# Performance work log

Hardware: AMD Instinct MI355X
Metric: run time of the kernel (lower is better)

Reference implementation:

```python
import jax, jax.numpy as jnp
import numpy as np

SPIKE_THRESHOLD = 0.5
SURROGATE_ALPHA = 4.0
EPS = 1e-8

B, S, D, F = 32, 8192, 64, 128


def _spike(x):
    # Heaviside spike with sigmoid surrogate (straight-through).
    hard = (x > 0).astype(x.dtype)
    soft = jax.nn.sigmoid(SURROGATE_ALPHA * x)
    return soft + jax.lax.stop_gradient(hard - soft)


def _kernel_features(x, kernel_weight):
    # phi(x) = exp(x) @ W  -> (B, S, F), as in LinearTransformerAttention._kernel_function
    return jnp.einsum('bsd,df->bsf', jnp.exp(x), kernel_weight)


def setup_inputs() -> dict:
    key = jax.random.key(0)
    k1, k2, k3, k4 = jax.random.split(key, 4)
    query = jax.random.normal(k1, (B, S, D), dtype=jnp.float32)
    key_t = jax.random.normal(k2, (B, S, D), dtype=jnp.float32)
    value = jax.random.normal(k3, (B, S, D), dtype=jnp.float32)
    # Xavier-uniform learned kernel map (head_dim -> num_features)
    limit = float(np.sqrt(6.0 / (D + F)))
    kernel_weight = jax.random.uniform(k4, (D, F), minval=-limit, maxval=limit, dtype=jnp.float32)
    return {"query": query, "key": key_t, "value": value, "kernel_weight": kernel_weight}


def reference(query, key, value, kernel_weight):
    # Kernel feature maps: (B, S, F)
    q_f = _kernel_features(query, kernel_weight)
    k_f = _kernel_features(key, kernel_weight)
    v_f = _kernel_features(value, kernel_weight)
    # Spiking threshold gating per time step on q/k features
    k_s = k_f * _spike(k_f - SPIKE_THRESHOLD)
    q_s = q_f * _spike(q_f - SPIKE_THRESHOLD)
    # Causal linear-attention via cumsum over time (dim=1)
    k_cum = jnp.cumsum(k_s, axis=1)
    kv_cum = jnp.cumsum(k_s * v_f, axis=1)
    attn = (kv_cum + EPS) / (k_cum + EPS)
    return q_s * attn  # (B, S, F)
```

## Files before the change

kernel.cpp:

```cpp
#include <hip/hip_runtime.h>


constexpr int cB = 32;
constexpr int cS = 8192;
constexpr int cD = 64;
constexpr int cF = 128;
constexpr int CHUNK = 64;
constexpr int NCH = cS / CHUNK;
constexpr int SLOT = 520;
constexpr int THR = 512;
constexpr int BPB = 16;
constexpr int ITERS = NCH / BPB;
constexpr float EPS_ = 1e-8f;

typedef __attribute__((ext_vector_type(8))) short bf16x8;
typedef __attribute__((ext_vector_type(4))) float f32x4;

#define MFMA16(a, b, c) __builtin_amdgcn_mfma_f32_16x16x32_bf16((a), (b), (c), 0, 0, 0)

__device__ __forceinline__ unsigned short bf16rn(float x) {
    unsigned u = __float_as_uint(x);
    unsigned r = u + 0x7FFFu + ((u >> 16) & 1u);
    return (unsigned short)(r >> 16);
}
__device__ __forceinline__ float bf16tof(unsigned short h) {
    return __uint_as_float((unsigned)h << 16);
}
__device__ __forceinline__ void split3(float x, unsigned short& a0,
                                       unsigned short& a1, unsigned short& a2) {
    a0 = bf16rn(x);
    float r1 = x - bf16tof(a0);
    a1 = bf16rn(r1);
    float r2 = r1 - bf16tof(a1);
    a2 = bf16rn(r2);
}
__device__ __forceinline__ unsigned cvtpk(float lo, float hi) {
    unsigned r;
    asm("v_cvt_pk_bf16_f32 %0, %1, %2" : "=v"(r) : "v"(lo), "v"(hi));
    return r;
}
__device__ __forceinline__ float unpk_lo(unsigned u) {
    return __uint_as_float(u << 16);
}
__device__ __forceinline__ float unpk_hi(unsigned u) {
    return __uint_as_float(u & 0xFFFF0000u);
}


__global__ __launch_bounds__(256) void k_wsplit(const float* __restrict__ W,
                                                unsigned short* __restrict__ ws) {
    for (int i = threadIdx.x; i < cD * cF; i += 256) {
        int d = i >> 7, f = i & 127;
        unsigned short s0, s1, s2;
        split3(W[i], s0, s1, s2);
        int n = f >> 4, k = d >> 5;
        int lane = (f & 15) | (((d >> 3) & 3) << 4);
        int j = d & 7;
        int base = ((n * 2 + k) * 3) * 512 + lane * 8 + j;
        ws[base]        = s0;
        ws[base + 512]  = s1;
        ws[base + 1024] = s2;
    }
}

__device__ __forceinline__ void transform_store(float4 a, int idx,
                                                unsigned short* __restrict__ af) {
    int row = idx >> 4, c4 = (idx & 15) * 4;
    float e0 = __expf(a.x), e1 = __expf(a.y), e2 = __expf(a.z), e3 = __expf(a.w);
    uint2 v0;
    v0.x = cvtpk(e0, e1);
    v0.y = cvtpk(e2, e3);
    float r0 = e0 - unpk_lo(v0.x), r1 = e1 - unpk_hi(v0.x);
    float r2 = e2 - unpk_lo(v0.y), r3 = e3 - unpk_hi(v0.y);
    uint2 v1;
    v1.x = cvtpk(r0, r1);
    v1.y = cvtpk(r2, r3);
    float t0 = r0 - unpk_lo(v1.x), t1 = r1 - unpk_hi(v1.x);
    float t2 = r2 - unpk_lo(v1.y), t3 = r3 - unpk_hi(v1.y);
    uint2 v2;
    v2.x = cvtpk(t0, t1);
    v2.y = cvtpk(t2, t3);

    int m = row >> 4, k = c4 >> 5;
    int lane_frag = (row & 15) | (((c4 >> 3) & 3) << 4);
    int jj = (c4 & 7) >> 2;
    int b0 = lane_frag * 16 + jj * 8;
    int byte = b0 ^ (((b0 >> 8) & 3) << 5);
    char* dst = (char*)af + (m * 2 + k) * 3 * (SLOT * 2) + byte;
    *(uint2*)(dst)            = v0;
    *(uint2*)(dst + SLOT * 2) = v1;
    *(uint2*)(dst + SLOT * 4) = v2;
}

__device__ __forceinline__ void load_mat(const float4* __restrict__ src, int t,
                                         float4 ld[2]) {
#pragma unroll
    for (int i = 0; i < 2; ++i) ld[i] = src[t + i * THR];
}
__device__ __forceinline__ void write_mat(const float4 ld[2],
                                          unsigned short* __restrict__ af, int t) {
    transform_store(ld[0], t, af);
    transform_store(ld[1], t + THR, af);
}

__device__ __forceinline__ void read_frag(const unsigned short* __restrict__ af,
                                          int mk, int l, bf16x8* out3) {
    int b0 = l * 16;
    int byte = b0 ^ (((b0 >> 8) & 3) << 5);
    const char* p = (const char*)af + mk * 3 * (SLOT * 2) + byte;
    out3[0] = *(const bf16x8*)(p);
    out3[1] = *(const bf16x8*)(p + SLOT * 2);
    out3[2] = *(const bf16x8*)(p + SLOT * 4);
}

#define GEMM6(acc, A, Wf)            \
    acc = MFMA16(A[0], Wf[0], acc);  \
    acc = MFMA16(A[0], Wf[1], acc);  \
    acc = MFMA16(A[1], Wf[0], acc);  \
    acc = MFMA16(A[1], Wf[1], acc);  \
    acc = MFMA16(A[0], Wf[2], acc);  \
    acc = MFMA16(A[2], Wf[0], acc);

__device__ __forceinline__ void gemm_pass(const unsigned short* __restrict__ af,
                                          const unsigned short* __restrict__ wsplit,
                                          int w, int l, f32x4 acc[4]) {
#pragma unroll
    for (int k = 0; k < 2; ++k) {
        bf16x8 wf[3];
#pragma unroll
        for (int p = 0; p < 3; ++p)
            wf[p] = *(const bf16x8*)(wsplit + (size_t)((((w * 2 + k) * 3 + p) * 512) + l * 8));
#pragma unroll
        for (int m = 0; m < 4; ++m) {
            bf16x8 a[3];
            read_frag(af, m * 2 + k, l, a);
            GEMM6(acc[m], a, wf);
        }
    }
}

__device__ __forceinline__ unsigned long long agg_ld(const unsigned long long* p) {
    return __hip_atomic_load(p, __ATOMIC_RELAXED, __HIP_MEMORY_SCOPE_AGENT);
}

__global__ __launch_bounds__(THR, 4) void k_main(const float* __restrict__ Q,
                                                 const float* __restrict__ K,
                                                 const float* __restrict__ V,
                                                 const unsigned short* __restrict__ wsplit,
                                                 float* __restrict__ out,
                                                 unsigned long long* __restrict__ agg)
{
    __shared__ unsigned short afK[24 * SLOT];
    __shared__ unsigned short afV[24 * SLOT];
    __shared__ unsigned short afQ[24 * SLOT];

    const int i0 = blockIdx.x;
    const int b = i0 >> 4, m = i0 & 15;
    const int t = threadIdx.x, w = t >> 6, l = t & 63;
    const int col = l & 15, g = l >> 4;
    const int fidx = w * 16 + col;

    float4 ldK[2], ldV[2], ldQ[2];
    {
        const size_t rb = ((size_t)b * cS + (size_t)m * CHUNK) * cD;
        load_mat((const float4*)(K + rb), t, ldK);
        load_mat((const float4*)(V + rb), t, ldV);
        load_mat((const float4*)(Q + rb), t, ldQ);
    }
    float carK = 0.f, carV = 0.f;

    for (int j = 0; j < ITERS; ++j) {
        const int c = j * BPB + m;

        __syncthreads();
        write_mat(ldK, afK, t);
        write_mat(ldV, afV, t);
        write_mat(ldQ, afQ, t);
        if (j + 1 < ITERS) {
            const size_t rb = ((size_t)b * cS + (size_t)(c + BPB) * CHUNK) * cD;
            load_mat((const float4*)(K + rb), t, ldK);
            load_mat((const float4*)(V + rb), t, ldV);
            load_mat((const float4*)(Q + rb), t, ldQ);
        }
        __syncthreads();

        f32x4 accK[4] = {};
        f32x4 accV[4] = {};
        gemm_pass(afK, wsplit, w, l, accK);
        gemm_pass(afV, wsplit, w, l, accV);

#pragma unroll
        for (int mm = 0; mm < 4; ++mm)
#pragma unroll
            for (int r = 0; r < 4; ++r) {
                float kf = accK[mm][r];
                float ks = (kf > 0.5f) ? kf : 0.f;
                accK[mm][r] = ks;
                accV[mm][r] = ks * accV[mm][r];
            }

        float ktot, kvtot;
        {
            float cK = 0.f, cV = 0.f;
#pragma unroll
            for (int mm = 0; mm < 4; ++mm) {
                f32x4 aK = accK[mm], aV = accV[mm];
                aK[1] += aK[0]; aK[2] += aK[1]; aK[3] += aK[2];
                aV[1] += aV[0]; aV[2] += aV[1]; aV[3] += aV[2];
                float tK = aK[3], tV = aV[3];
                float uK = __shfl_up(tK, 16), uV = __shfl_up(tV, 16);
                if (g >= 1) { tK += uK; tV += uV; }
                float xK = __shfl_up(tK, 32), xV = __shfl_up(tV, 32);
                if (g >= 2) { tK += xK; tV += xV; }
                float eK = tK - aK[3] + cK;
                float eV = tV - aV[3] + cV;
                aK[0] += eK; aK[1] += eK; aK[2] += eK; aK[3] += eK;
                aV[0] += eV; aV[1] += eV; aV[2] += eV; aV[3] += eV;
                accK[mm] = aK; accV[mm] = aV;
                cK += __shfl(tK, 48 + col);
                cV += __shfl(tV, 48 + col);
            }
            ktot = cK; kvtot = cV;
        }

        if (g == 0) {
            unsigned long long u = ((unsigned long long)__float_as_uint(kvtot) << 32)
                                 | (unsigned long long)__float_as_uint(ktot + 1.0f);
            __hip_atomic_store(agg + (size_t)(b * NCH + c) * cF + fidx, u,
                               __ATOMIC_RELAXED, __HIP_MEMORY_SCOPE_AGENT);
        }

        {
            const int lastc = (j == 0) ? -1 : (c - BPB);
            float dk = 0.f, dv = 0.f;
            const unsigned long long* base = agg + (size_t)b * NCH * cF + fidx;
            for (int cc = c - 1 - g; cc > lastc; cc -= 4) {
                const unsigned long long* p = base + (size_t)cc * cF;
                unsigned long long v0 = agg_ld(p);
                while ((unsigned)v0 == 0u) v0 = agg_ld(p);
                dk += __uint_as_float((unsigned)v0) - 1.0f;
                dv += __uint_as_float((unsigned)(v0 >> 32));
            }
            dk += __shfl_xor(dk, 16);
            dk += __shfl_xor(dk, 32);
            dv += __shfl_xor(dv, 16);
            dv += __shfl_xor(dv, 32);
            carK += dk;
            carV += dv;
        }

#pragma unroll
        for (int mm = 0; mm < 4; ++mm)
#pragma unroll
            for (int r = 0; r < 4; ++r) {
                float kc = accK[mm][r] + carK;
                float vc = accV[mm][r] + carV;
                accV[mm][r] = __fdividef(vc + EPS_, kc + EPS_);
            }
        carK += ktot;
        carV += kvtot;

        f32x4 accQ[4] = {};
        gemm_pass(afQ, wsplit, w, l, accQ);

        const size_t obase = ((size_t)b * cS + (size_t)c * CHUNK) * cF;
#pragma unroll
        for (int mm = 0; mm < 4; ++mm)
#pragma unroll
            for (int r = 0; r < 4; ++r) {
                int s = mm * 16 + g * 4 + r;
                float qf = accQ[mm][r];
                float qs = (qf > 0.5f) ? qf : 0.f;
                out[obase + (size_t)s * cF + fidx] = qs * accV[mm][r];
            }
    }
}

extern "C" void kernel_launch(void* const* d_in, const int* in_sizes, int n_in,
                              void* d_out, int out_size, void* d_ws, size_t ws_size,
                              hipStream_t stream) {
    const float* q = (const float*)d_in[0];
    const float* k = (const float*)d_in[1];
    const float* v = (const float*)d_in[2];
    const float* w = (const float*)d_in[3];
    float* out = (float*)d_out;

    unsigned short* wsplit = (unsigned short*)d_ws;
    unsigned long long* agg = (unsigned long long*)((char*)d_ws + 65536);

    hipMemsetAsync(agg, 0, (size_t)cB * NCH * cF * sizeof(unsigned long long), stream);
    k_wsplit<<<1, 256, 0, stream>>>(w, wsplit);
    k_main<<<cB * BPB, THR, 0, stream>>>(q, k, v, wsplit, out, agg);
}
```

Measured before the change: 142.3 us.

## Reuse K LDS buffer for Q, compute chunk totals early, prefetch aggregates

Drops the separate Q shared-memory buffer and stages Q into the K buffer after the K/V work, behind an extra pair of barriers, so LDS use falls and launch bounds rise from 4 to 6 blocks per CU. Chunk totals are now computed by a direct reduction and published before the in-chunk prefix scan, and the up-to-four predecessor aggregate loads are issued early so they overlap the scan instead of being polled serially. The cost is extra synchronisation and a later issue of the next-chunk global prefetch, which shortens the overlap of the loads, plus tighter register pressure under the higher occupancy target.

```diff
diff --git a/kernel.cpp b/kernel.cpp
--- a/kernel.cpp
+++ b/kernel.cpp
@@ -143,7 +143,7 @@
     return __hip_atomic_load(p, __ATOMIC_RELAXED, __HIP_MEMORY_SCOPE_AGENT);
 }
 
-__global__ __launch_bounds__(THR, 4) void k_main(const float* __restrict__ Q,
+__global__ __launch_bounds__(THR, 6) void k_main(const float* __restrict__ Q,
                                                  const float* __restrict__ K,
                                                  const float* __restrict__ V,
                                                  const unsigned short* __restrict__ wsplit,
@@ -152,7 +152,6 @@
 {
     __shared__ unsigned short afK[24 * SLOT];
     __shared__ unsigned short afV[24 * SLOT];
-    __shared__ unsigned short afQ[24 * SLOT];
 
     const int i0 = blockIdx.x;
     const int b = i0 >> 4, m = i0 & 15;
@@ -175,13 +174,6 @@
         __syncthreads();
         write_mat(ldK, afK, t);
         write_mat(ldV, afV, t);
-        write_mat(ldQ, afQ, t);
-        if (j + 1 < ITERS) {
-            const size_t rb = ((size_t)b * cS + (size_t)(c + BPB) * CHUNK) * cD;
-            load_mat((const float4*)(K + rb), t, ldK);
-            load_mat((const float4*)(V + rb), t, ldV);
-            load_mat((const float4*)(Q + rb), t, ldQ);
-        }
         __syncthreads();
 
         f32x4 accK[4] = {};
@@ -199,7 +191,35 @@
                 accV[mm][r] = ks * accV[mm][r];
             }
 
-        float ktot, kvtot;
+        float ktot = 0.f, kvtot = 0.f;
+#pragma unroll
+        for (int mm = 0; mm < 4; ++mm)
+#pragma unroll
+            for (int r = 0; r < 4; ++r) {
+                ktot += accK[mm][r];
+                kvtot += accV[mm][r];
+            }
+        ktot += __shfl_xor(ktot, 16);
+        ktot += __shfl_xor(ktot, 32);
+        kvtot += __shfl_xor(kvtot, 16);
+        kvtot += __shfl_xor(kvtot, 32);
+        if (g == 0) {
+            unsigned long long u = ((unsigned long long)__float_as_uint(kvtot) << 32)
+                                 | (unsigned long long)__float_as_uint(ktot + 1.0f);
+            __hip_atomic_store(agg + (size_t)(b * NCH + c) * cF + fidx, u,
+                               __ATOMIC_RELAXED, __HIP_MEMORY_SCOPE_AGENT);
+        }
+
+        const int lastc = (j == 0) ? -1 : (c - BPB);
+        const int cc0 = c - 1 - g;
+        const unsigned long long* base = agg + (size_t)b * NCH * cF + fidx;
+        unsigned long long vv[4];
+#pragma unroll
+        for (int s2 = 0; s2 < 4; ++s2) {
+            int cc = cc0 - 4 * s2;
+            vv[s2] = (cc > lastc) ? agg_ld(base + (size_t)cc * cF) : 0ull;
+        }
+
         {
             float cK = 0.f, cV = 0.f;
 #pragma unroll
@@ -220,26 +240,19 @@
                 cK += __shfl(tK, 48 + col);
                 cV += __shfl(tV, 48 + col);
             }
-            ktot = cK; kvtot = cV;
-        }
-
-        if (g == 0) {
-            unsigned long long u = ((unsigned long long)__float_as_uint(kvtot) << 32)
-                                 | (unsigned long long)__float_as_uint(ktot + 1.0f);
-            __hip_atomic_store(agg + (size_t)(b * NCH + c) * cF + fidx, u,
-                               __ATOMIC_RELAXED, __HIP_MEMORY_SCOPE_AGENT);
         }
 
         {
-            const int lastc = (j == 0) ? -1 : (c - BPB);
             float dk = 0.f, dv = 0.f;
-            const unsigned long long* base = agg + (size_t)b * NCH * cF + fidx;
-            for (int cc = c - 1 - g; cc > lastc; cc -= 4) {
-                const unsigned long long* p = base + (size_t)cc * cF;
-                unsigned long long v0 = agg_ld(p);
-                while ((unsigned)v0 == 0u) v0 = agg_ld(p);
-                dk += __uint_as_float((unsigned)v0) - 1.0f;
-                dv += __uint_as_float((unsigned)(v0 >> 32));
+#pragma unroll
+            for (int s2 = 0; s2 < 4; ++s2) {
+                int cc = cc0 - 4 * s2;
+                if (cc > lastc) {
+                    unsigned long long v0 = vv[s2];
+                    while ((unsigned)v0 == 0u) v0 = agg_ld(base + (size_t)cc * cF);
+                    dk += __uint_as_float((unsigned)v0) - 1.0f;
+                    dv += __uint_as_float((unsigned)(v0 >> 32));
+                }
             }
             dk += __shfl_xor(dk, 16);
             dk += __shfl_xor(dk, 32);
@@ -260,8 +273,18 @@
         carK += ktot;
         carV += kvtot;
 
+        __syncthreads();
+        write_mat(ldQ, afK, t);
+        if (j + 1 < ITERS) {
+            const size_t rb = ((size_t)b * cS + (size_t)(c + BPB) * CHUNK) * cD;
+            load_mat((const float4*)(K + rb), t, ldK);
+            load_mat((const float4*)(V + rb), t, ldV);
+            load_mat((const float4*)(Q + rb), t, ldQ);
+        }
+        __syncthreads();
+
         f32x4 accQ[4] = {};
-        gemm_pass(afQ, wsplit, w, l, accQ);
+        gemm_pass(afK, wsplit, w, l, accQ);
 
         const size_t obase = ((size_t)b * cS + (size_t)c * CHUNK) * cF;
 #pragma unroll
```

Result: slower. 247.7 us (+74.1%).

## Use contiguous per-block chunk ranges with a single cross-block carry exchange

Applied to the files above, without the earlier changes.

Each block now handles 8 contiguous chunks instead of chunks strided across blocks. A first pass computes K/V features and local prefix sums, staging them as packed fp16 pairs in the output buffer. One carry exchange per block then replaces the per-chunk chain of spin-waits on the aggregate buffer. A second pass computes the Q features and reads back the staged prefixes to form the output. This removes the serial cross-block dependency on every chunk, at the cost of an extra write and read of the output buffer, and fp16 storage of the running cumulative sums costs precision.

```diff
diff --git a/kernel.cpp b/kernel.cpp
--- a/kernel.cpp
+++ b/kernel.cpp
@@ -1,4 +1,5 @@
 #include <hip/hip_runtime.h>
+#include <hip/hip_fp16.h>
 
 
 constexpr int cB = 32;
@@ -6,11 +7,10 @@
 constexpr int cD = 64;
 constexpr int cF = 128;
 constexpr int CHUNK = 64;
-constexpr int NCH = cS / CHUNK;
 constexpr int SLOT = 520;
 constexpr int THR = 512;
 constexpr int BPB = 16;
-constexpr int ITERS = NCH / BPB;
+constexpr int CPB = 8;
 constexpr float EPS_ = 1e-8f;
 
 typedef __attribute__((ext_vector_type(8))) short bf16x8;
@@ -150,9 +150,8 @@
                                                  float* __restrict__ out,
                                                  unsigned long long* __restrict__ agg)
 {
-    __shared__ unsigned short afK[24 * SLOT];
-    __shared__ unsigned short afV[24 * SLOT];
-    __shared__ unsigned short afQ[24 * SLOT];
+    __shared__ unsigned short afA[24 * SLOT];
+    __shared__ unsigned short afB[24 * SLOT];
 
     const int i0 = blockIdx.x;
     const int b = i0 >> 4, m = i0 & 15;
@@ -160,34 +159,28 @@
     const int col = l & 15, g = l >> 4;
     const int fidx = w * 16 + col;
 
-    float4 ldK[2], ldV[2], ldQ[2];
-    {
-        const size_t rb = ((size_t)b * cS + (size_t)m * CHUNK) * cD;
-        load_mat((const float4*)(K + rb), t, ldK);
-        load_mat((const float4*)(V + rb), t, ldV);
-        load_mat((const float4*)(Q + rb), t, ldQ);
-    }
-    float carK = 0.f, carV = 0.f;
-
-    for (int j = 0; j < ITERS; ++j) {
-        const int c = j * BPB + m;
-
+    const size_t blockrow = (size_t)b * cS + (size_t)m * (CPB * CHUNK);
+
+    float4 ldK[2], ldV[2];
+    load_mat((const float4*)(K + blockrow * cD), t, ldK);
+    load_mat((const float4*)(V + blockrow * cD), t, ldV);
+    float Pk = 0.f, Pv = 0.f;
+
+    for (int j = 0; j < CPB; ++j) {
         __syncthreads();
-        write_mat(ldK, afK, t);
-        write_mat(ldV, afV, t);
-        write_mat(ldQ, afQ, t);
-        if (j + 1 < ITERS) {
-            const size_t rb = ((size_t)b * cS + (size_t)(c + BPB) * CHUNK) * cD;
+        write_mat(ldK, afA, t);
+        write_mat(ldV, afB, t);
+        if (j + 1 < CPB) {
+            const size_t rb = (blockrow + (size_t)(j + 1) * CHUNK) * cD;
             load_mat((const float4*)(K + rb), t, ldK);
             load_mat((const float4*)(V + rb), t, ldV);
-            load_mat((const float4*)(Q + rb), t, ldQ);
         }
         __syncthreads();
 
         f32x4 accK[4] = {};
         f32x4 accV[4] = {};
-        gemm_pass(afK, wsplit, w, l, accK);
-        gemm_pass(afV, wsplit, w, l, accV);
+        gemm_pass(afA, wsplit, w, l, accK);
+        gemm_pass(afB, wsplit, w, l, accV);
 
 #pragma unroll
         for (int mm = 0; mm < 4; ++mm)
@@ -199,79 +192,95 @@
                 accV[mm][r] = ks * accV[mm][r];
             }
 
-        float ktot, kvtot;
-        {
-            float cK = 0.f, cV = 0.f;
-#pragma unroll
-            for (int mm = 0; mm < 4; ++mm) {
-                f32x4 aK = accK[mm], aV = accV[mm];
-                aK[1] += aK[0]; aK[2] += aK[1]; aK[3] += aK[2];
-                aV[1] += aV[0]; aV[2] += aV[1]; aV[3] += aV[2];
-                float tK = aK[3], tV = aV[3];
-                float uK = __shfl_up(tK, 16), uV = __shfl_up(tV, 16);
-                if (g >= 1) { tK += uK; tV += uV; }
-                float xK = __shfl_up(tK, 32), xV = __shfl_up(tV, 32);
-                if (g >= 2) { tK += xK; tV += xV; }
-                float eK = tK - aK[3] + cK;
-                float eV = tV - aV[3] + cV;
-                aK[0] += eK; aK[1] += eK; aK[2] += eK; aK[3] += eK;
-                aV[0] += eV; aV[1] += eV; aV[2] += eV; aV[3] += eV;
-                accK[mm] = aK; accV[mm] = aV;
-                cK += __shfl(tK, 48 + col);
-                cV += __shfl(tV, 48 + col);
-            }
-            ktot = cK; kvtot = cV;
-        }
-
-        if (g == 0) {
-            unsigned long long u = ((unsigned long long)__float_as_uint(kvtot) << 32)
-                                 | (unsigned long long)__float_as_uint(ktot + 1.0f);
-            __hip_atomic_store(agg + (size_t)(b * NCH + c) * cF + fidx, u,
-                               __ATOMIC_RELAXED, __HIP_MEMORY_SCOPE_AGENT);
-        }
-
-        {
-            const int lastc = (j == 0) ? -1 : (c - BPB);
-            float dk = 0.f, dv = 0.f;
-            const unsigned long long* base = agg + (size_t)b * NCH * cF + fidx;
-            for (int cc = c - 1 - g; cc > lastc; cc -= 4) {
-                const unsigned long long* p = base + (size_t)cc * cF;
-                unsigned long long v0 = agg_ld(p);
-                while ((unsigned)v0 == 0u) v0 = agg_ld(p);
-                dk += __uint_as_float((unsigned)v0) - 1.0f;
-                dv += __uint_as_float((unsigned)(v0 >> 32));
-            }
-            dk += __shfl_xor(dk, 16);
-            dk += __shfl_xor(dk, 32);
-            dv += __shfl_xor(dv, 16);
-            dv += __shfl_xor(dv, 32);
-            carK += dk;
-            carV += dv;
-        }
-
-#pragma unroll
-        for (int mm = 0; mm < 4; ++mm)
-#pragma unroll
-            for (int r = 0; r < 4; ++r) {
-                float kc = accK[mm][r] + carK;
-                float vc = accV[mm][r] + carV;
-                accV[mm][r] = __fdividef(vc + EPS_, kc + EPS_);
-            }
-        carK += ktot;
-        carV += kvtot;
-
-        f32x4 accQ[4] = {};
-        gemm_pass(afQ, wsplit, w, l, accQ);
-
-        const size_t obase = ((size_t)b * cS + (size_t)c * CHUNK) * cF;
+        float cK = 0.f, cV = 0.f;
+#pragma unroll
+        for (int mm = 0; mm < 4; ++mm) {
+            f32x4 aK = accK[mm], aV = accV[mm];
+            aK[1] += aK[0]; aK[2] += aK[1]; aK[3] += aK[2];
+            aV[1] += aV[0]; aV[2] += aV[1]; aV[3] += aV[2];
+            float tK = aK[3], tV = aV[3];
+            float uK = __shfl_up(tK, 16), uV = __shfl_up(tV, 16);
+            if (g >= 1) { tK += uK; tV += uV; }
+            float xK = __shfl_up(tK, 32), xV = __shfl_up(tV, 32);
+            if (g >= 2) { tK += xK; tV += xV; }
+            float eK = tK - aK[3] + cK;
+            float eV = tV - aV[3] + cV;
+            aK[0] += eK; aK[1] += eK; aK[2] += eK; aK[3] += eK;
+            aV[0] += eV; aV[1] += eV; aV[2] += eV; aV[3] += eV;
+            accK[mm] = aK; accV[mm] = aV;
+            cK += __shfl(tK, 48 + col);
+            cV += __shfl(tV, 48 + col);
+        }
+
+        const size_t obase = (blockrow + (size_t)j * CHUNK) * cF;
 #pragma unroll
         for (int mm = 0; mm < 4; ++mm)
 #pragma unroll
             for (int r = 0; r < 4; ++r) {
                 int s = mm * 16 + g * 4 + r;
+                __half2 h2;
+                h2.x = __float2half(accK[mm][r] + Pk);
+                h2.y = __float2half(accV[mm][r] + Pv);
+                out[obase + (size_t)s * cF + fidx] = __uint_as_float(*(unsigned*)&h2);
+            }
+        Pk += cK;
+        Pv += cV;
+    }
+
+    if (g == 0) {
+        unsigned long long u = ((unsigned long long)__float_as_uint(Pv) << 32)
+                             | (unsigned long long)__float_as_uint(Pk + 1.0f);
+        __hip_atomic_store(agg + (size_t)(b * BPB + m) * cF + fidx, u,
+                           __ATOMIC_RELAXED, __HIP_MEMORY_SCOPE_AGENT);
+    }
+    float carK, carV;
+    {
+        float dk = 0.f, dv = 0.f;
+        const unsigned long long* base = agg + (size_t)b * BPB * cF + fidx;
+        for (int mm = m - 1 - g; mm >= 0; mm -= 4) {
+            const unsigned long long* p = base + (size_t)mm * cF;
+            unsigned long long v0 = agg_ld(p);
+            while ((unsigned)v0 == 0u) v0 = agg_ld(p);
+            dk += __uint_as_float((unsigned)v0) - 1.0f;
+            dv += __uint_as_float((unsigned)(v0 >> 32));
+        }
+        dk += __shfl_xor(dk, 16);
+        dk += __shfl_xor(dk, 32);
+        dv += __shfl_xor(dv, 16);
+        dv += __shfl_xor(dv, 32);
+        carK = dk;
+        carV = dv;
+    }
+
+    float4 ldQ[2];
+    load_mat((const float4*)(Q + blockrow * cD), t, ldQ);
+    for (int j = 0; j < CPB; ++j) {
+        __syncthreads();
+        write_mat(ldQ, afA, t);
+        if (j + 1 < CPB) {
+            const size_t rb = (blockrow + (size_t)(j + 1) * CHUNK) * cD;
+            load_mat((const float4*)(Q + rb), t, ldQ);
+        }
+        __syncthreads();
+
+        f32x4 accQ[4] = {};
+        gemm_pass(afA, wsplit, w, l, accQ);
+
+        const size_t obase = (blockrow + (size_t)j * CHUNK) * cF;
+#pragma unroll
+        for (int mm = 0; mm < 4; ++mm)
+#pragma unroll
+            for (int r = 0; r < 4; ++r) {
+                int s = mm * 16 + g * 4 + r;
+                const size_t idx = obase + (size_t)s * cF + fidx;
+                float pf = out[idx];
+                __half2 h2 = *(__half2*)&pf;
+                float kc = __half2float(h2.x) + carK;
+                float vc = __half2float(h2.y) + carV;
+                float attn = __fdividef(vc + EPS_, kc + EPS_);
                 float qf = accQ[mm][r];
                 float qs = (qf > 0.5f) ? qf : 0.f;
-                out[obase + (size_t)s * cF + fidx] = qs * accV[mm][r];
+                out[idx] = qs * attn;
             }
     }
 }
@@ -288,7 +297,7 @@
     unsigned short* wsplit = (unsigned short*)d_ws;
     unsigned long long* agg = (unsigned long long*)((char*)d_ws + 65536);
 
-    hipMemsetAsync(agg, 0, (size_t)cB * NCH * cF * sizeof(unsigned long long), stream);
+    hipMemsetAsync(agg, 0, (size_t)cB * BPB * cF * sizeof(unsigned long long), stream);
     k_wsplit<<<1, 256, 0, stream>>>(w, wsplit);
     k_main<<<cB * BPB, THR, 0, stream>>>(q, k, v, wsplit, out, agg);
 }
```

Measured after the change: 177.5 us. +24.7%, slower.
